# Optimization experiments

Measured on AMD Instinct MI355X. Metric: run time of the kernel, lower is better.

Reference implementation:

```python
import jax, jax.numpy as jnp
import numpy as np

DIM = 1024
HEADS = 16
HEAD_DIM = 64
INNER = HEADS * HEAD_DIM  # 1024


def setup_inputs() -> dict:
    key = jax.random.key(0)
    ks = jax.random.split(key, 7)
    b, n, m = 2, 2048, 2048
    s = 0.02
    return {
        "x": jax.random.normal(ks[0], (b, n, DIM), dtype=jnp.float32),
        "context": jax.random.normal(ks[1], (b, m, DIM), dtype=jnp.float32),
        "w_kv": jax.random.normal(ks[2], (DIM, 2 * INNER), dtype=jnp.float32) * s,
        "w_q": jax.random.normal(ks[3], (DIM, INNER), dtype=jnp.float32) * s,
        "w_out1": jax.random.normal(ks[4], (INNER, DIM), dtype=jnp.float32) * s,
        "w_out2": jax.random.normal(ks[5], (DIM, DIM), dtype=jnp.float32) * s,
        "gamma": jnp.ones((DIM,), dtype=jnp.float32),
    }


def _split_heads(t):
    # [b, n, h*d] -> [b, h, n, d]
    b, n, _ = t.shape
    return t.reshape(b, n, HEADS, HEAD_DIM).transpose(0, 2, 1, 3)


def reference(x, context, w_kv, w_q, w_out1, w_out2, gamma):
    scale = HEAD_DIM ** -0.5
    kv = context @ w_kv                      # [b, m, 2*inner]
    k, v = jnp.split(kv, 2, axis=-1)
    q = _split_heads(x @ w_q)                # [b, h, n, d]
    k = _split_heads(k)                      # [b, h, m, d]
    v = _split_heads(v)
    dots = jnp.einsum('bhid,bhjd->bhij', q, k) * scale
    attn = jax.nn.softmax(dots, axis=-1)
    out = jnp.einsum('bhij,bhjd->bhid', attn, v)
    b, h, n, d = out.shape
    out = out.transpose(0, 2, 1, 3).reshape(b, n, h * d)   # [b, n, inner]
    out = jax.nn.relu(out @ w_out1) @ w_out2               # to_out MLP (dropout off)
    # AttnLayerNorm: layer_norm over last dim with gamma, beta=0
    mean = jnp.mean(out, axis=-1, keepdims=True)
    var = jnp.var(out, axis=-1, keepdims=True)
    return (out - mean) * jax.lax.rsqrt(var + 1e-5) * gamma
```

## Files before the change

kernel.cpp:

```cpp
#include <hip/hip_runtime.h>
#include <hip/hip_bf16.h>

typedef unsigned short u16;
typedef unsigned int u32;
typedef __attribute__((ext_vector_type(4))) float f32x4;
typedef __attribute__((ext_vector_type(16))) float f32x16;
typedef __attribute__((ext_vector_type(8))) __bf16 bf16x8;

constexpr int kDim   = 1024;
constexpr int kSeq   = 2048;
constexpr int kB     = 2;
constexpr int kHeads = 16;
constexpr int kRows  = kB * kSeq;

__device__ __forceinline__ u16 f2bf(float f) {
  __hip_bfloat16 h = __float2bfloat16(f);
  return __builtin_bit_cast(u16, h);
}

__device__ __forceinline__ u32 pkbf(float a, float b) {
  return (u32)f2bf(a) | ((u32)f2bf(b) << 16);
}

__device__ __forceinline__ u32 cvtpk(float lo, float hi) {
  u32 r;
  asm("v_cvt_pk_bf16_f32 %0, %1, %2" : "=v"(r) : "v"(lo), "v"(hi));
  return r;
}

__device__ __forceinline__ float exp2x(float x) {
#if __has_builtin(__builtin_amdgcn_exp2f)
  return __builtin_amdgcn_exp2f(x);
#else
  return exp2f(x);
#endif
}

__device__ __forceinline__ void plswap(u32& a, u32& b) {
  asm volatile("v_permlane32_swap_b32 %0, %1" : "+v"(a), "+v"(b));
}

__device__ __forceinline__ float xsum32(float x) {
  return x + __shfl_xor(x, 32);
}

__device__ __forceinline__ void gload_lds16(const void* src, void* dst) {
  __builtin_amdgcn_global_load_lds(
      (const __attribute__((address_space(1))) void*)src,
      (__attribute__((address_space(3))) void*)dst, 16, 0, 0);
}

__device__ __forceinline__ f32x4 mfma16(bf16x8 a, bf16x8 b, f32x4 c) {
  return __builtin_amdgcn_mfma_f32_16x16x32_bf16(a, b, c, 0, 0, 0);
}

__device__ __forceinline__ f32x16 mfma32(bf16x8 a, bf16x8 b, f32x16 c) {
  return __builtin_amdgcn_mfma_f32_32x32x16_bf16(a, b, c, 0, 0, 0);
}

__device__ __forceinline__ void convert_body(const float* __restrict__ in,
                                             u16* __restrict__ out, int n4,
                                             int vbid, int nblk) {
  int i = vbid * 256 + threadIdx.x;
  const int stride = nblk * 256;
  for (; i < n4; i += stride) {
    float4 v = ((const float4*)in)[i];
    ushort4 o;
    o.x = f2bf(v.x); o.y = f2bf(v.y); o.z = f2bf(v.z); o.w = f2bf(v.w);
    ((ushort4*)out)[i] = o;
  }
}

__device__ __forceinline__ void transpose_tile(const float* __restrict__ in,
                                               u16* __restrict__ out, int K, int N,
                                               int bx, int by, float (*tile)[33]) {
  const int tx = threadIdx.x & 31;
  const int ty = threadIdx.x >> 5;
  const int k0 = by * 32;
  const int n0 = bx * 32;
#pragma unroll
  for (int i = 0; i < 4; ++i)
    tile[ty + i * 8][tx] = in[(size_t)(k0 + ty + i * 8) * N + n0 + tx];
  __syncthreads();
#pragma unroll
  for (int i = 0; i < 4; ++i)
    out[(size_t)(n0 + ty + i * 8) * K + k0 + tx] = f2bf(tile[tx][ty + i * 8]);
}

__global__ __launch_bounds__(256) void prep_kernel(
    const float* __restrict__ x,   u16* __restrict__ xb,
    const float* __restrict__ ctx, u16* __restrict__ cb,
    const float* __restrict__ wkv, u16* __restrict__ wkvT,
    const float* __restrict__ wq,  u16* __restrict__ wqT,
    const float* __restrict__ w1,  u16* __restrict__ w1T,
    const float* __restrict__ w2,  u16* __restrict__ w2T) {
  __shared__ float tile[32][33];
  int bid = blockIdx.x;
  if (bid < 2048) { transpose_tile(wkv, wkvT, 1024, 2048, bid & 63, bid >> 6, tile); return; }
  bid -= 2048;
  if (bid < 1024) { transpose_tile(wq, wqT, 1024, 1024, bid & 31, bid >> 5, tile); return; }
  bid -= 1024;
  if (bid < 1024) { transpose_tile(w1, w1T, 1024, 1024, bid & 31, bid >> 5, tile); return; }
  bid -= 1024;
  if (bid < 1024) { transpose_tile(w2, w2T, 1024, 1024, bid & 31, bid >> 5, tile); return; }
  bid -= 1024;
  if (bid < 1024) { convert_body(x, xb, kRows * 1024 / 4, bid, 1024); return; }
  bid -= 1024;
  convert_body(ctx, cb, kRows * 1024 / 4, bid, 1024);
}

template <int EPI, int TN>
__device__ __forceinline__ void gemm_body(const u16* __restrict__ A,
                                          const u16* __restrict__ Bt,
                                          void* __restrict__ out0,
                                          void* __restrict__ out1, int N,
                                          int m0, int n0,
                                          u16* ldsA, u16* ldsB) {
  constexpr int K  = 1024;
  constexpr int WN = (TN == 128) ? 2 : 1;
  constexpr int WM = 4 / WN;
  constexpr int MF = 128 / WM / 16;
  constexpr int NF = TN / WN / 16;
  constexpr int NCHUNK = 16 + TN / 8;
  constexpr int CPW = NCHUNK / 4;
  const int tid  = threadIdx.x;
  const int lane = tid & 63;
  const int wave = tid >> 6;
  const int wm = wave / WN, wn = wave % WN;

  f32x4 acc[MF][NF];
#pragma unroll
  for (int i = 0; i < MF; ++i)
#pragma unroll
    for (int j = 0; j < NF; ++j) acc[i][j] = (f32x4)0.f;

  const int srow = lane >> 3;
  const int sslt = lane & 7;

  for (int kt = 0; kt < K / 64; ++kt) {
    const int k0 = kt * 64;
#pragma unroll
    for (int i = 0; i < CPW; ++i) {
      const int c = wave * CPW + i;
      if (c < 16) {
        const int row = c * 8 + srow;
        const int cb  = sslt ^ (row & 7);
        gload_lds16(A + (size_t)(m0 + row) * K + k0 + cb * 8, ldsA + c * 512);
      } else {
        const int cc  = c - 16;
        const int row = cc * 8 + srow;
        const int cb  = sslt ^ (row & 7);
        gload_lds16(Bt + (size_t)(n0 + row) * K + k0 + cb * 8, ldsB + cc * 512);
      }
    }
    __syncthreads();
#pragma unroll
    for (int ks = 0; ks < 2; ++ks) {
      const int kb = (ks * 32 + (lane >> 4) * 8) >> 3;
      bf16x8 af[MF], bfr[NF];
#pragma unroll
      for (int mf = 0; mf < MF; ++mf) {
        const int row = wm * (128 / WM) + mf * 16 + (lane & 15);
        af[mf] = *(const bf16x8*)(ldsA + row * 64 + (kb ^ (row & 7)) * 8);
      }
#pragma unroll
      for (int nf = 0; nf < NF; ++nf) {
        const int row = wn * (TN / WN) + nf * 16 + (lane & 15);
        bfr[nf] = *(const bf16x8*)(ldsB + row * 64 + (kb ^ (row & 7)) * 8);
      }
#pragma unroll
      for (int mf = 0; mf < MF; ++mf)
#pragma unroll
        for (int nf = 0; nf < NF; ++nf)
          acc[mf][nf] = mfma16(af[mf], bfr[nf], acc[mf][nf]);
    }
    __syncthreads();
  }

  const int rb = (lane >> 4) * 4;
  const int cc = lane & 15;
#pragma unroll
  for (int mf = 0; mf < MF; ++mf)
#pragma unroll
    for (int nf = 0; nf < NF; ++nf)
#pragma unroll
      for (int r = 0; r < 4; ++r) {
        const int grow = m0 + wm * (128 / WM) + mf * 16 + rb + r;
        const int gcol = n0 + wn * (TN / WN) + nf * 16 + cc;
        const float v = acc[mf][nf][r];
        if constexpr (EPI == 1) {
          ((u16*)out0)[(size_t)grow * N + gcol] = f2bf(v * 0.18033688f);
        } else if constexpr (EPI == 2) {
          ((u16*)out0)[(size_t)grow * N + gcol] = f2bf(v > 0.f ? v : 0.f);
        } else if constexpr (EPI == 3) {
          ((float*)out0)[(size_t)grow * N + gcol] = v;
        } else {
          const int b = grow >> 11, m = grow & 2047;
          if (gcol < 1024) {
            ((u16*)out0)[(size_t)grow * 1024 + gcol] = f2bf(v);
          } else {
            const int df = gcol - 1024;
            const int h = df >> 6, d = df & 63;
            ((u16*)out1)[(((size_t)(b * kHeads + h) * 64 + d) << 11) + m] = f2bf(v);
          }
        }
      }
}

template <int EPI, int TN>
__global__ __launch_bounds__(256) void gemm_bt(const u16* __restrict__ A,
                                               const u16* __restrict__ Bt,
                                               void* __restrict__ out0,
                                               void* __restrict__ out1, int N) {
  __shared__ u16 ldsA[128 * 64];
  __shared__ u16 ldsB[TN * 64];
  const int nwg = gridDim.x * gridDim.y;
  int bid = blockIdx.y * gridDim.x + blockIdx.x;
  bid = (bid & 7) * (nwg >> 3) + (bid >> 3);
  const int m0 = (bid / gridDim.x) * 128;
  const int n0 = (bid % gridDim.x) * TN;
  gemm_body<EPI, TN>(A, Bt, out0, out1, N, m0, n0, ldsA, ldsB);
}

__global__ __launch_bounds__(256, 3) void gemm_kvq(const u16* __restrict__ cb,
                                                   const u16* __restrict__ wkvT,
                                                   u16* __restrict__ kbuf,
                                                   u16* __restrict__ vT,
                                                   const u16* __restrict__ xb,
                                                   const u16* __restrict__ wqT,
                                                   u16* __restrict__ qbuf) {
  __shared__ u16 ldsA[128 * 64];
  __shared__ u16 ldsB[128 * 64];
  const int swz = (blockIdx.x & 7) * 128 + (blockIdx.x >> 3);
  const int chunk = swz >> 7, off = swz & 127;
  if (off < 64) {
    const int bid = chunk * 64 + off;
    gemm_body<4, 128>(cb, wkvT, kbuf, vT, 2048,
                      (bid >> 4) * 128, (bid & 15) * 128, ldsA, ldsB);
  } else {
    const int bid = chunk * 64 + (off - 64);
    gemm_body<1, 64>(xb, wqT, qbuf, nullptr, 1024,
                     (bid >> 4) * 128, (bid & 15) * 64, ldsA, ldsB);
  }
}

__global__ __launch_bounds__(512, 4) void attn_kernel(const u16* __restrict__ Q,
                                                      const u16* __restrict__ Kb,
                                                      const u16* __restrict__ Vt,
                                                      u16* __restrict__ O) {
  __shared__ __align__(16) unsigned char smem[65536];

  const int swz = (blockIdx.x & 7) * 64 + (blockIdx.x >> 3);
  const int qt = swz & 15;
  const int bh = swz >> 4;
  const int h = bh & 15, b = bh >> 4;

  const int tid  = threadIdx.x;
  const int lane = tid & 63;
  const int wave = tid >> 6;
  const int kw   = wave & 1;
  const int qw   = wave >> 1;
  const int l32  = lane & 31;
  const int hi   = lane >> 5;
  const int q0   = qt * 128 + qw * 32;

  const u16* qp = Q + (size_t)(b * kSeq + q0 + l32) * 1024 + h * 64 + hi * 8;
  bf16x8 bq[4];
#pragma unroll
  for (int ks = 0; ks < 4; ++ks) bq[ks] = *(const bf16x8*)(qp + ks * 16);

  f32x16 acc[2];
  acc[0] = (f32x16)0.f; acc[1] = (f32x16)0.f;
  float l_ = 0.f;

  const int srow = lane >> 3, sslt = lane & 7;

  auto stage_pair = [&](int dbuf, int kvbase) {
    u16* baseK = (u16*)(smem + dbuf * 32768);
    u16* baseV = (u16*)(smem + dbuf * 32768 + 16384);
#pragma unroll
    for (int j = 0; j < 4; ++j) {
      const int c = wave * 4 + j;
      if (c < 16) {
        const int par = c >> 3, cc = c & 7;
        const int row = cc * 8 + srow;
        const int cb  = sslt ^ (row & 7);
        gload_lds16(Kb + (size_t)(b * kSeq + kvbase + par * 64 + row) * 1024 +
                        h * 64 + cb * 8,
                    baseK + par * 4096 + cc * 512);
      } else {
        const int cv = c - 16, par = cv >> 3, cc = cv & 7;
        const int row = cc * 8 + srow;
        const int cb  = sslt ^ (row & 7);
        gload_lds16(Vt + (size_t)((b * kHeads + h) * 64 + row) * kSeq +
                        kvbase + par * 64 + cb * 8,
                    baseV + par * 4096 + cc * 512);
      }
    }
  };

  stage_pair(0, 0);

  for (int it = 0; it < kSeq / 128; ++it) {
    __syncthreads();
    const int cur = it & 1;
    if (it + 1 < kSeq / 128) stage_pair(cur ^ 1, (it + 1) * 128);

    const u16* myK = (const u16*)(smem + cur * 32768) + kw * 4096;
    const u16* myV = (const u16*)(smem + cur * 32768 + 16384) + kw * 4096;

#pragma unroll
    for (int kvt = 0; kvt < 2; ++kvt) {
      const int krow = kvt * 32 + l32;
      const int ksw  = krow & 7;
      bf16x8 kf[4];
#pragma unroll
      for (int ks = 0; ks < 4; ++ks)
        kf[ks] = *(const bf16x8*)(&myK[krow * 64 + ((2 * ks + hi) ^ ksw) * 8]);
      f32x16 s = (f32x16)0.f;
#pragma unroll
      for (int ks = 0; ks < 4; ++ks) s = mfma32(kf[ks], bq[ks], s);

#pragma unroll
      for (int r = 0; r < 16; ++r) s[r] = exp2x(s[r]);
      const float t0 = (s[0] + s[1]) + (s[2] + s[3]);
      const float t1 = (s[4] + s[5]) + (s[6] + s[7]);
      const float t2 = (s[8] + s[9]) + (s[10] + s[11]);
      const float t3 = (s[12] + s[13]) + (s[14] + s[15]);
      l_ += (t0 + t1) + (t2 + t3);

      u32 w[8];
#pragma unroll
      for (int p = 0; p < 8; ++p) w[p] = cvtpk(s[2 * p], s[2 * p + 1]);
      plswap(w[0], w[2]); plswap(w[1], w[3]);
      plswap(w[4], w[6]); plswap(w[5], w[7]);
      union { u32 u[4]; bf16x8 v; } f0, f1;
      f0.u[0] = w[0]; f0.u[1] = w[1]; f0.u[2] = w[2]; f0.u[3] = w[3];
      f1.u[0] = w[4]; f1.u[1] = w[5]; f1.u[2] = w[6]; f1.u[3] = w[7];

#pragma unroll
      for (int nd = 0; nd < 2; ++nd) {
        const int vrow = nd * 32 + l32;
        const int vsw  = vrow & 7;
        bf16x8 v0 = *(const bf16x8*)(&myV[vrow * 64 + ((4 * kvt + hi) ^ vsw) * 8]);
        bf16x8 v1 = *(const bf16x8*)(&myV[vrow * 64 + ((4 * kvt + 2 + hi) ^ vsw) * 8]);
        acc[nd] = mfma32(v0, f0.v, acc[nd]);
        acc[nd] = mfma32(v1, f1.v, acc[nd]);
      }
    }
  }

  __syncthreads();
  float* mg = (float*)smem;
  if (kw == 1) {
    float* mp = mg + (qw * 64 + lane) * 33;
#pragma unroll
    for (int r = 0; r < 16; ++r) { mp[r] = acc[0][r]; mp[16 + r] = acc[1][r]; }
    mp[32] = l_;
  }
  __syncthreads();
  if (kw == 0) {
    const float* mp = mg + (qw * 64 + lane) * 33;
#pragma unroll
    for (int r = 0; r < 16; ++r) { acc[0][r] += mp[r]; acc[1][r] += mp[16 + r]; }
    l_ += mp[32];

    const float inv = 1.f / xsum32(l_);
    const size_t rowb = (size_t)(b * kSeq + q0 + l32) * 1024 + h * 64;
#pragma unroll
    for (int nd = 0; nd < 2; ++nd)
#pragma unroll
      for (int r4 = 0; r4 < 4; ++r4) {
        uint2 o;
        o.x = pkbf(acc[nd][4 * r4 + 0] * inv, acc[nd][4 * r4 + 1] * inv);
        o.y = pkbf(acc[nd][4 * r4 + 2] * inv, acc[nd][4 * r4 + 3] * inv);
        *(uint2*)(O + rowb + nd * 32 + r4 * 8 + hi * 4) = o;
      }
  }
}

__global__ __launch_bounds__(256) void ln_kernel(float* __restrict__ io,
                                                 const float* __restrict__ gamma) {
  const int row = blockIdx.x;
  float* p = io + (size_t)row * 1024;
  float4 v = ((const float4*)p)[threadIdx.x];
  float s  = v.x + v.y + v.z + v.w;
  float ss = v.x * v.x + v.y * v.y + v.z * v.z + v.w * v.w;
#pragma unroll
  for (int m = 1; m < 64; m <<= 1) {
    s  += __shfl_xor(s, m);
    ss += __shfl_xor(ss, m);
  }
  __shared__ float red[8];
  const int wave = threadIdx.x >> 6, lane = threadIdx.x & 63;
  if (lane == 0) { red[wave] = s; red[4 + wave] = ss; }
  __syncthreads();
  s  = red[0] + red[1] + red[2] + red[3];
  ss = red[4] + red[5] + red[6] + red[7];
  const float mean = s * (1.f / 1024.f);
  const float var  = ss * (1.f / 1024.f) - mean * mean;
  const float rr   = rsqrtf(var + 1e-5f);
  float4 g = ((const float4*)gamma)[threadIdx.x];
  v.x = (v.x - mean) * rr * g.x;
  v.y = (v.y - mean) * rr * g.y;
  v.z = (v.z - mean) * rr * g.z;
  v.w = (v.w - mean) * rr * g.w;
  ((float4*)p)[threadIdx.x] = v;
}

extern "C" void kernel_launch(void* const* d_in, const int* in_sizes, int n_in,
                              void* d_out, int out_size, void* d_ws, size_t ws_size,
                              hipStream_t stream) {
  const float* x      = (const float*)d_in[0];
  const float* ctx    = (const float*)d_in[1];
  const float* w_kv   = (const float*)d_in[2];
  const float* w_q    = (const float*)d_in[3];
  const float* w_out1 = (const float*)d_in[4];
  const float* w_out2 = (const float*)d_in[5];
  const float* gamma  = (const float*)d_in[6];

  char* ws = (char*)d_ws;
  size_t off = 0;
  auto alloc = [&](size_t bytes) {
    void* p = ws + off;
    off += (bytes + 255) & ~(size_t)255;
    return p;
  };
  u16* xb   = (u16*)alloc((size_t)kRows * 1024 * 2);
  u16* cb   = (u16*)alloc((size_t)kRows * 1024 * 2);
  u16* wkvT = (u16*)alloc((size_t)2048 * 1024 * 2);
  u16* wqT  = (u16*)alloc((size_t)1024 * 1024 * 2);
  u16* w1T  = (u16*)alloc((size_t)1024 * 1024 * 2);
  u16* w2T  = (u16*)alloc((size_t)1024 * 1024 * 2);
  u16* kbuf = (u16*)alloc((size_t)kRows * 1024 * 2);
  u16* vT   = (u16*)alloc((size_t)kRows * 1024 * 2);
  u16* qbuf = (u16*)alloc((size_t)kRows * 1024 * 2);
  u16* attno  = cb;
  u16* hidden = xb;

  prep_kernel<<<7168, 256, 0, stream>>>(x, xb, ctx, cb, w_kv, wkvT, w_q, wqT,
                                        w_out1, w1T, w_out2, w2T);
  gemm_kvq<<<1024, 256, 0, stream>>>(cb, wkvT, kbuf, vT, xb, wqT, qbuf);
  attn_kernel<<<512, 512, 0, stream>>>(qbuf, kbuf, vT, attno);
  gemm_bt<2, 64><<<dim3(1024 / 64, kRows / 128), 256, 0, stream>>>(attno, w1T, hidden, nullptr, 1024);
  gemm_bt<3, 64><<<dim3(1024 / 64, kRows / 128), 256, 0, stream>>>(hidden, w2T, d_out, nullptr, 1024);
  ln_kernel<<<kRows, 256, 0, stream>>>((float*)d_out, gamma);
}
```

Baseline: 135.1 us.

## Use 64x64 tiled MLP GEMMs and compute softmax row sums via MFMA

```diff
diff --git a/kernel.cpp b/kernel.cpp
--- a/kernel.cpp
+++ b/kernel.cpp
@@ -38,10 +38,6 @@
 
 __device__ __forceinline__ void plswap(u32& a, u32& b) {
   asm volatile("v_permlane32_swap_b32 %0, %1" : "+v"(a), "+v"(b));
-}
-
-__device__ __forceinline__ float xsum32(float x) {
-  return x + __shfl_xor(x, 32);
 }
 
 __device__ __forceinline__ void gload_lds16(const void* src, void* dst) {
@@ -190,10 +186,6 @@
         const float v = acc[mf][nf][r];
         if constexpr (EPI == 1) {
           ((u16*)out0)[(size_t)grow * N + gcol] = f2bf(v * 0.18033688f);
-        } else if constexpr (EPI == 2) {
-          ((u16*)out0)[(size_t)grow * N + gcol] = f2bf(v > 0.f ? v : 0.f);
-        } else if constexpr (EPI == 3) {
-          ((float*)out0)[(size_t)grow * N + gcol] = v;
         } else {
           const int b = grow >> 11, m = grow & 2047;
           if (gcol < 1024) {
@@ -205,21 +197,6 @@
           }
         }
       }
-}
-
-template <int EPI, int TN>
-__global__ __launch_bounds__(256) void gemm_bt(const u16* __restrict__ A,
-                                               const u16* __restrict__ Bt,
-                                               void* __restrict__ out0,
-                                               void* __restrict__ out1, int N) {
-  __shared__ u16 ldsA[128 * 64];
-  __shared__ u16 ldsB[TN * 64];
-  const int nwg = gridDim.x * gridDim.y;
-  int bid = blockIdx.y * gridDim.x + blockIdx.x;
-  bid = (bid & 7) * (nwg >> 3) + (bid >> 3);
-  const int m0 = (bid / gridDim.x) * 128;
-  const int n0 = (bid % gridDim.x) * TN;
-  gemm_body<EPI, TN>(A, Bt, out0, out1, N, m0, n0, ldsA, ldsB);
 }
 
 __global__ __launch_bounds__(256, 3) void gemm_kvq(const u16* __restrict__ cb,
@@ -244,6 +221,65 @@
   }
 }
 
+template <int EPI>
+__global__ __launch_bounds__(256, 4) void gemm64(const u16* __restrict__ A,
+                                                 const u16* __restrict__ Bt,
+                                                 void* __restrict__ out0, int N) {
+  constexpr int K = 1024;
+  __shared__ u16 ldsA[64 * 64];
+  __shared__ u16 ldsB[64 * 64];
+  const int lane = threadIdx.x & 63;
+  const int wave = threadIdx.x >> 6;
+  const int l31  = lane & 31;
+  const int hi   = lane >> 5;
+  const int wm = wave >> 1, wn = wave & 1;
+
+  const int swz = (blockIdx.x & 7) * 128 + (blockIdx.x >> 3);
+  const int m0 = (swz >> 4) * 64;
+  const int n0 = (swz & 15) * 64;
+
+  f32x16 acc = (f32x16)0.f;
+
+  const int srow = lane >> 3, sslt = lane & 7;
+  const int arow = wm * 32 + l31;
+  const int brow = wn * 32 + l31;
+  const int asw = arow & 7, bsw = brow & 7;
+
+  for (int kt = 0; kt < K / 64; ++kt) {
+    const int k0 = kt * 64;
+#pragma unroll
+    for (int j = 0; j < 4; ++j) {
+      const int c = wave * 4 + j;
+      const int row = (c & 7) * 8 + srow;
+      const int cb  = sslt ^ (row & 7);
+      if (c < 8)
+        gload_lds16(A + (size_t)(m0 + row) * K + k0 + cb * 8, ldsA + (c & 7) * 512);
+      else
+        gload_lds16(Bt + (size_t)(n0 + row) * K + k0 + cb * 8, ldsB + (c & 7) * 512);
+    }
+    __syncthreads();
+#pragma unroll
+    for (int ks = 0; ks < 4; ++ks) {
+      bf16x8 af = *(const bf16x8*)(ldsA + arow * 64 + ((2 * ks + hi) ^ asw) * 8);
+      bf16x8 bf = *(const bf16x8*)(ldsB + brow * 64 + ((2 * ks + hi) ^ bsw) * 8);
+      acc = mfma32(af, bf, acc);
+    }
+    __syncthreads();
+  }
+
+#pragma unroll
+  for (int r = 0; r < 16; ++r) {
+    const int grow = m0 + wm * 32 + (r & 3) + 8 * (r >> 2) + 4 * hi;
+    const int gcol = n0 + wn * 32 + l31;
+    const float v = acc[r];
+    if constexpr (EPI == 2) {
+      ((u16*)out0)[(size_t)grow * N + gcol] = f2bf(v > 0.f ? v : 0.f);
+    } else {
+      ((float*)out0)[(size_t)grow * N + gcol] = v;
+    }
+  }
+}
+
 __global__ __launch_bounds__(512, 4) void attn_kernel(const u16* __restrict__ Q,
                                                       const u16* __restrict__ Kb,
                                                       const u16* __restrict__ Vt,
@@ -269,9 +305,13 @@
 #pragma unroll
   for (int ks = 0; ks < 4; ++ks) bq[ks] = *(const bf16x8*)(qp + ks * 16);
 
+  union { u32 u[4]; bf16x8 v; } ones;
+#pragma unroll
+  for (int i = 0; i < 4; ++i) ones.u[i] = 0x3F803F80;
+
   f32x16 acc[2];
   acc[0] = (f32x16)0.f; acc[1] = (f32x16)0.f;
-  float l_ = 0.f;
+  f32x16 accl = (f32x16)0.f;
 
   const int srow = lane >> 3, sslt = lane & 7;
 
@@ -318,16 +358,13 @@
       for (int ks = 0; ks < 4; ++ks)
         kf[ks] = *(const bf16x8*)(&myK[krow * 64 + ((2 * ks + hi) ^ ksw) * 8]);
       f32x16 s = (f32x16)0.f;
+      __builtin_amdgcn_s_setprio(1);
 #pragma unroll
       for (int ks = 0; ks < 4; ++ks) s = mfma32(kf[ks], bq[ks], s);
+      __builtin_amdgcn_s_setprio(0);
 
 #pragma unroll
       for (int r = 0; r < 16; ++r) s[r] = exp2x(s[r]);
-      const float t0 = (s[0] + s[1]) + (s[2] + s[3]);
-      const float t1 = (s[4] + s[5]) + (s[6] + s[7]);
-      const float t2 = (s[8] + s[9]) + (s[10] + s[11]);
-      const float t3 = (s[12] + s[13]) + (s[14] + s[15]);
-      l_ += (t0 + t1) + (t2 + t3);
 
       u32 w[8];
 #pragma unroll
@@ -338,18 +375,23 @@
       f0.u[0] = w[0]; f0.u[1] = w[1]; f0.u[2] = w[2]; f0.u[3] = w[3];
       f1.u[0] = w[4]; f1.u[1] = w[5]; f1.u[2] = w[6]; f1.u[3] = w[7];
 
-#pragma unroll
-      for (int nd = 0; nd < 2; ++nd) {
-        const int vrow = nd * 32 + l32;
-        const int vsw  = vrow & 7;
-        bf16x8 v0 = *(const bf16x8*)(&myV[vrow * 64 + ((4 * kvt + hi) ^ vsw) * 8]);
-        bf16x8 v1 = *(const bf16x8*)(&myV[vrow * 64 + ((4 * kvt + 2 + hi) ^ vsw) * 8]);
-        acc[nd] = mfma32(v0, f0.v, acc[nd]);
-        acc[nd] = mfma32(v1, f1.v, acc[nd]);
-      }
-    }
-  }
-
+      const int vsw0 = l32 & 7, vsw1 = (32 + l32) & 7;
+      bf16x8 v00 = *(const bf16x8*)(&myV[l32 * 64 + ((4 * kvt + hi) ^ vsw0) * 8]);
+      bf16x8 v01 = *(const bf16x8*)(&myV[l32 * 64 + ((4 * kvt + 2 + hi) ^ vsw0) * 8]);
+      bf16x8 v10 = *(const bf16x8*)(&myV[(32 + l32) * 64 + ((4 * kvt + hi) ^ vsw1) * 8]);
+      bf16x8 v11 = *(const bf16x8*)(&myV[(32 + l32) * 64 + ((4 * kvt + 2 + hi) ^ vsw1) * 8]);
+      __builtin_amdgcn_s_setprio(1);
+      acc[0] = mfma32(v00, f0.v, acc[0]);
+      acc[0] = mfma32(v01, f1.v, acc[0]);
+      acc[1] = mfma32(v10, f0.v, acc[1]);
+      acc[1] = mfma32(v11, f1.v, acc[1]);
+      accl   = mfma32(ones.v, f0.v, accl);
+      accl   = mfma32(ones.v, f1.v, accl);
+      __builtin_amdgcn_s_setprio(0);
+    }
+  }
+
+  const float l_ = accl[0];
   __syncthreads();
   float* mg = (float*)smem;
   if (kw == 1) {
@@ -361,11 +403,11 @@
   __syncthreads();
   if (kw == 0) {
     const float* mp = mg + (qw * 64 + lane) * 33;
+    float lsum = l_ + mp[32];
 #pragma unroll
     for (int r = 0; r < 16; ++r) { acc[0][r] += mp[r]; acc[1][r] += mp[16 + r]; }
-    l_ += mp[32];
-
-    const float inv = 1.f / xsum32(l_);
+
+    const float inv = 1.f / lsum;
     const size_t rowb = (size_t)(b * kSeq + q0 + l32) * 1024 + h * 64;
 #pragma unroll
     for (int nd = 0; nd < 2; ++nd)
@@ -442,7 +484,7 @@
                                         w_out1, w1T, w_out2, w2T);
   gemm_kvq<<<1024, 256, 0, stream>>>(cb, wkvT, kbuf, vT, xb, wqT, qbuf);
   attn_kernel<<<512, 512, 0, stream>>>(qbuf, kbuf, vT, attno);
-  gemm_bt<2, 64><<<dim3(1024 / 64, kRows / 128), 256, 0, stream>>>(attno, w1T, hidden, nullptr, 1024);
-  gemm_bt<3, 64><<<dim3(1024 / 64, kRows / 128), 256, 0, stream>>>(hidden, w2T, d_out, nullptr, 1024);
+  gemm64<2><<<1024, 256, 0, stream>>>(attno, w1T, hidden, 1024);
+  gemm64<3><<<1024, 256, 0, stream>>>(hidden, w2T, d_out, 1024);
   ln_kernel<<<kRows, 256, 0, stream>>>((float*)d_out, gamma);
 }
```

Measured after the change: 135.4 us. About the same (+0.2%).
